# Performance work log

Measured on AMD Instinct MI355X. Metric: run time of the kernel, lower is better.

Reference implementation:

```python
import jax, jax.numpy as jnp
import numpy as np

NEG_SLOPE = 0.1
BN_EPS = 1e-5
STD_EPS = 1e-5


def leaky_relu(x):
    return jnp.where(x >= 0, x, NEG_SLOPE * x)


def conv_bn_act(x, w, gamma, beta):
    # Conv1d(kernel_size=1, bias=False) + BatchNorm1d (train-mode batch stats) + LeakyReLU(0.1)
    y = jnp.einsum('bcn,oc->bon', x, w)
    m = y.mean(axis=(0, 2), keepdims=True)
    v = y.var(axis=(0, 2), keepdims=True)  # biased, as torch BN
    y = (y - m) / jnp.sqrt(v + BN_EPS) * gamma[None, :, None] + beta[None, :, None]
    return leaky_relu(y)


def knn_idx(x, k):
    # x: [B, C, N]; faithful to torch knn(): topk(k+1) of negative squared distance, then keep first k (includes self)
    xx = jnp.sum(x * x, axis=1, keepdims=True)            # [B, 1, N]
    inner = -2.0 * jnp.einsum('bcn,bcm->bnm', x, x)       # [B, N, N]
    pd = -xx - inner - jnp.swapaxes(xx, 1, 2)             # [B, N, N]
    _, idx = jax.lax.top_k(pd, k + 1)
    return idx[:, :, :k]


def setup_inputs() -> dict:
    key = jax.random.key(0)
    ks = jax.random.split(key, 4)
    B, C, N, O = 8, 3, 4096, 32
    return {
        'xyz': jax.random.normal(ks[0], (B, C, N), dtype=jnp.float32),
        'w_nn': jax.random.normal(ks[1], (O, C), dtype=jnp.float32) * 0.1,
        'alpha': jnp.ones((1, 1, 1, O), dtype=jnp.float32),
        'beta_a': jnp.zeros((1, 1, 1, O), dtype=jnp.float32),
        'w0': jax.random.normal(ks[2], (O, C), dtype=jnp.float32) * 0.1,
        'g0': jnp.ones((O,), dtype=jnp.float32),
        'b0': jnp.zeros((O,), dtype=jnp.float32),
        'w1': jax.random.normal(ks[3], (O, O), dtype=jnp.float32) * 0.1,
        'g1': jnp.ones((O,), dtype=jnp.float32),
        'b1': jnp.zeros((O,), dtype=jnp.float32),
        'k': 16,
    }


def reference(xyz, w_nn, alpha, beta_a, w0, g0, b0, w1, g1, b1, k):
    # MLP branch on raw channels
    x = conv_bn_act(xyz, w0, g0, b0)
    x = conv_bn_act(x, w1, g1, b1)          # [B, 32, N]

    # KNN + gather neighbors
    idx = knn_idx(xyz, k)                   # [B, N, k]
    pts = jnp.swapaxes(xyz, 1, 2)           # [B, N, C]
    grouped = jax.vmap(lambda p, i: p[i])(pts, idx)  # [B, N, k, C]

    # neighbor_normal: diff -> 1x1 conv -> global-std normalize -> affine
    res = grouped - pts[:, :, None, :]
    res = jnp.einsum('bnkc,oc->bnko', res, w_nn)      # [B, N, k, 32]
    B = res.shape[0]
    std = jnp.std(res.reshape(B, -1), axis=-1, ddof=1).reshape(B, 1, 1, 1)  # torch.std is unbiased
    gp = alpha * (res / (std + STD_EPS)) + beta_a

    # max over neighbors, to [B, 32, N]
    gp = jnp.swapaxes(gp.max(axis=2), 1, 2)

    point_feature = jnp.concatenate([x, gp], axis=1)  # [B, 64, N]
    return point_feature, idx
```

## Files before the change

### kernel.cpp

```cpp
#include <hip/hip_runtime.h>
#include <stdint.h>

#define B_  8
#define N_  4096
#define O_  32
#define K_  16
#define BN_ (B_ * N_)
#define PF_ (B_ * 64 * N_)
#define CB_ 256
#define RPB 4
#define CHK 512
#define NCHK (N_ / CHK)

enum : int {
  WS_PARTA = 0,
  WS_XX    = 1024,
  WS_SC0   = WS_XX + BN_,
  WS_SH0   = WS_SC0 + 32,
  WS_PARTC = WS_SH0 + 32,
  WS_SC1   = WS_PARTC + 4096,
  WS_SH1   = WS_SC1 + 32,
  WS_MAXV  = WS_SH1 + 32,
  WS_MINV  = WS_MAXV + BN_ * 32,
  WS_ROWS  = WS_MINV + BN_ * 32,
  WS_DEN   = WS_ROWS + BN_ * 2,
  WS_TOTAL = WS_DEN + 8
};
#define WS_PARTC2 WS_MAXV

__global__ __launch_bounds__(256) void kA(const float* __restrict__ xyz,
                                          float* __restrict__ ws) {
  int tid = threadIdx.x;
  int gid = blockIdx.x * 256 + tid;
  float s0 = 0.f, s1 = 0.f, s2 = 0.f;
  float m00 = 0.f, m01 = 0.f, m02 = 0.f, m11 = 0.f, m12 = 0.f, m22 = 0.f;
  for (int i = gid; i < BN_; i += 64 * 256) {
    int b = i >> 12, n = i & (N_ - 1);
    const float* xb = xyz + b * 3 * N_;
    float x0 = xb[n], x1 = xb[N_ + n], x2 = xb[2 * N_ + n];
    float xx = __fadd_rn(__fadd_rn(__fmul_rn(x0, x0), __fmul_rn(x1, x1)),
                         __fmul_rn(x2, x2));
    ws[WS_XX + i] = xx;
    s0 += x0; s1 += x1; s2 += x2;
    m00 = fmaf(x0, x0, m00); m01 = fmaf(x0, x1, m01); m02 = fmaf(x0, x2, m02);
    m11 = fmaf(x1, x1, m11); m12 = fmaf(x1, x2, m12); m22 = fmaf(x2, x2, m22);
  }
  __shared__ float sd[256];
  float acc[9] = {s0, s1, s2, m00, m01, m02, m11, m12, m22};
#pragma unroll
  for (int q = 0; q < 9; ++q) {
    sd[tid] = acc[q];
    __syncthreads();
    for (int s = 128; s > 0; s >>= 1) {
      if (tid < s) sd[tid] += sd[tid + s];
      __syncthreads();
    }
    if (tid == 0) ws[WS_PARTA + blockIdx.x * 9 + q] = sd[0];
    __syncthreads();
  }
}

__global__ __launch_bounds__(256) void kC(const float* __restrict__ xyz,
                                          const float* __restrict__ w0,
                                          const float* __restrict__ g0,
                                          const float* __restrict__ b0,
                                          const float* __restrict__ w1,
                                          float* __restrict__ ws) {
  __shared__ float S9[9];
  __shared__ float w0s[96], sc0s[32], sh0s[32], w1s[32 * 33], xs[8][33], red[256];
  int tid = threadIdx.x;
  if (tid < 9) {
    float s = 0.f;
    for (int blk = 0; blk < 64; ++blk) s += ws[WS_PARTA + blk * 9 + tid];
    S9[tid] = s;
  }
  if (tid < 96) w0s[tid] = w0[tid];
  for (int i = tid; i < 1024; i += 256) w1s[(i >> 5) * 33 + (i & 31)] = w1[i];
  __syncthreads();
  if (tid < 32) {
    const float inv = 1.0f / 32768.0f;
    float mc0 = S9[0] * inv, mc1 = S9[1] * inv, mc2 = S9[2] * inv;
    float M00 = S9[3] * inv, M01 = S9[4] * inv, M02 = S9[5] * inv;
    float M11 = S9[6] * inv, M12 = S9[7] * inv, M22 = S9[8] * inv;
    float w0c = w0[tid * 3], w1c = w0[tid * 3 + 1], w2c = w0[tid * 3 + 2];
    float m = w0c * mc0 + w1c * mc1 + w2c * mc2;
    float e2 = w0c * w0c * M00 + w1c * w1c * M11 + w2c * w2c * M22 +
               2.f * (w0c * w1c * M01 + w0c * w2c * M02 + w1c * w2c * M12);
    float v = fmaxf(e2 - m * m, 0.f);
    float sc = g0[tid] / sqrtf(v + 1e-5f);
    float sh = b0[tid] - m * sc;
    sc0s[tid] = sc; sh0s[tid] = sh;
    if (blockIdx.x == 0) { ws[WS_SC0 + tid] = sc; ws[WS_SH0 + tid] = sh; }
  }
  __syncthreads();
  int p = tid >> 5, o = tid & 31;
  float S = 0.f, S2 = 0.f;
  for (int it = 0; it < 16; ++it) {
    int i = blockIdx.x * 128 + it * 8 + p;
    int b = i >> 12, n = i & (N_ - 1);
    const float* xb = xyz + b * 3 * N_;
    float x0 = xb[n], x1 = xb[N_ + n], x2 = xb[2 * N_ + n];
    float y0 = x0 * w0s[o * 3] + x1 * w0s[o * 3 + 1] + x2 * w0s[o * 3 + 2];
    float a = y0 * sc0s[o] + sh0s[o];
    xs[p][o] = (a >= 0.f) ? a : 0.1f * a;
    __syncthreads();
    float y1 = 0.f;
#pragma unroll
    for (int c = 0; c < 32; ++c) y1 = fmaf(w1s[o * 33 + c], xs[p][c], y1);
    S += y1; S2 = fmaf(y1, y1, S2);
    __syncthreads();
  }
  red[tid] = S;
  __syncthreads();
  if (p == 0) {
    float t = 0.f;
    for (int pp = 0; pp < 8; ++pp) t += red[pp * 32 + o];
    ws[WS_PARTC2 + blockIdx.x * 64 + o] = t;
  }
  __syncthreads();
  red[tid] = S2;
  __syncthreads();
  if (p == 0) {
    float t = 0.f;
    for (int pp = 0; pp < 8; ++pp) t += red[pp * 32 + o];
    ws[WS_PARTC2 + blockIdx.x * 64 + 32 + o] = t;
  }
}

__global__ __launch_bounds__(256) void kE(const float* __restrict__ xyz,
                                          const float* __restrict__ w0,
                                          const float* __restrict__ w1,
                                          const float* __restrict__ g1,
                                          const float* __restrict__ b1,
                                          const float* __restrict__ ws,
                                          float* __restrict__ out) {
  __shared__ float w0s[96], sc0s[32], sh0s[32], sc1s[32], sh1s[32], w1s[32 * 33],
      xs[8][33];
  int tid = threadIdx.x;
  if (tid < 96) w0s[tid] = w0[tid];
  if (tid < 32) {
    sc0s[tid] = ws[WS_SC0 + tid]; sh0s[tid] = ws[WS_SH0 + tid];
    float S = 0.f, S2 = 0.f;
    for (int blk = 0; blk < CB_; ++blk) {
      S += ws[WS_PARTC2 + blk * 64 + tid];
      S2 += ws[WS_PARTC2 + blk * 64 + 32 + tid];
    }
    float m = S / 32768.f;
    float v = fmaxf(S2 / 32768.f - m * m, 0.f);
    float sc = g1[tid] / sqrtf(v + 1e-5f);
    sc1s[tid] = sc; sh1s[tid] = b1[tid] - m * sc;
  }
  for (int i = tid; i < 1024; i += 256) w1s[(i >> 5) * 33 + (i & 31)] = w1[i];
  __syncthreads();
  int p = tid >> 5, o = tid & 31;
  int o2 = tid >> 3, p2 = tid & 7;
  for (int it = 0; it < 16; ++it) {
    int i = blockIdx.x * 128 + it * 8 + p;
    int b = i >> 12, n = i & (N_ - 1);
    const float* xb = xyz + b * 3 * N_;
    float x0 = xb[n], x1 = xb[N_ + n], x2 = xb[2 * N_ + n];
    float y0 = x0 * w0s[o * 3] + x1 * w0s[o * 3 + 1] + x2 * w0s[o * 3 + 2];
    float a = y0 * sc0s[o] + sh0s[o];
    xs[p][o] = (a >= 0.f) ? a : 0.1f * a;
    __syncthreads();
    float y1 = 0.f;
#pragma unroll
    for (int c = 0; c < 32; ++c) y1 = fmaf(w1s[o * 33 + c], xs[p][c], y1);
    float z = y1 * sc1s[o] + sh1s[o];
    float x1v = (z >= 0.f) ? z : 0.1f * z;
    __syncthreads();
    xs[p][o] = x1v;
    __syncthreads();
    int i2 = blockIdx.x * 128 + it * 8 + p2;
    int b2 = i2 >> 12, n2 = i2 & (N_ - 1);
    out[b2 * 64 * N_ + o2 * N_ + n2] = xs[p2][o2];
    __syncthreads();
  }
}

__global__ __launch_bounds__(256) void kF(const float* __restrict__ xyz,
                                          const float* __restrict__ w_nn,
                                          float* __restrict__ out,
                                          float* __restrict__ ws) {
  int tid = threadIdx.x;
  int wave = tid >> 6, lane = tid & 63;
  int row = blockIdx.x * RPB + wave;
  int b = row >> 12, n = row & (N_ - 1);
  const float* xb = xyz + b * 3 * N_;
  const float* xxp = ws + WS_XX + b * N_;
  float qx = xb[n], qy = xb[N_ + n], qz = xb[2 * N_ + n];
  float xxn = xxp[n];

  __shared__ float sx[2][CHK], sy[2][CHK], sz[2][CHK];
  __shared__ unsigned long long list[RPB][64];
  __shared__ float rb[RPB][16][33];

  float keys[64];
  float mn = __builtin_inff();
  float rx0, rx1, ry0, ry1, rz0, rz1;
  rx0 = xb[tid];           rx1 = xb[tid + 256];
  ry0 = xb[N_ + tid];      ry1 = xb[N_ + tid + 256];
  rz0 = xb[2 * N_ + tid];  rz1 = xb[2 * N_ + tid + 256];
#pragma unroll
  for (int c = 0; c < NCHK; ++c) {
    int buf = c & 1;
    sx[buf][tid] = rx0;  sx[buf][tid + 256] = rx1;
    sy[buf][tid] = ry0;  sy[buf][tid + 256] = ry1;
    sz[buf][tid] = rz0;  sz[buf][tid + 256] = rz1;
    __syncthreads();
    if (c + 1 < NCHK) {
      int i0 = (c + 1) * CHK + tid;
      rx0 = xb[i0];           rx1 = xb[i0 + 256];
      ry0 = xb[N_ + i0];      ry1 = xb[N_ + i0 + 256];
      rz0 = xb[2 * N_ + i0];  rz1 = xb[2 * N_ + i0 + 256];
    }
#pragma unroll
    for (int jj = 0; jj < CHK / 64; ++jj) {
      int ml = (jj << 6) | lane;
      float px = sx[buf][ml], py = sy[buf][ml], pz = sz[buf][ml];
      float m0 = __fmul_rn(px, px);
      float m1 = __fmul_rn(py, py);
      float m2 = __fmul_rn(pz, pz);
      asm volatile("" : "+v"(m0), "+v"(m1), "+v"(m2));
      float pw = __fadd_rn(__fadd_rn(m0, m1), m2);
      asm volatile("" : "+v"(pw));
      float dot = __fmaf_rn(pz, qz, __fmaf_rn(py, qy, __fmul_rn(px, qx)));
      asm volatile("" : "+v"(dot));
      float inner = __fmul_rn(-2.0f, dot);
      float t = __fsub_rn(-pw, inner);
      float pn = __fsub_rn(xxn, t);
      keys[c * (CHK / 64) + jj] = pn;
      mn = fminf(mn, pn);
    }
    __syncthreads();
  }

  unsigned e;
  {
    unsigned u = __float_as_uint(mn);
    u ^= ((unsigned)((int)u >> 31)) | 0x80000000u;
    e = u;
  }
#pragma unroll
  for (int k = 2; k <= 64; k <<= 1) {
#pragma unroll
    for (int d = k >> 1; d >= 1; d >>= 1) {
      unsigned pe = __shfl_xor(e, d, 64);
      bool up = ((lane & k) == 0);
      bool lower = ((lane & d) == 0);
      unsigned lo = (e < pe) ? e : pe;
      unsigned hi = (e < pe) ? pe : e;
      e = (up == lower) ? lo : hi;
    }
  }
  unsigned tm = __shfl(e, 15, 64);
  unsigned tfu = (tm & 0x80000000u) ? (tm ^ 0x80000000u) : ~tm;
  float T = __uint_as_float(tfu);

  list[wave][lane] = ~0ull;
  __syncthreads();
  int base = 0;
#pragma unroll
  for (int j = 0; j < 64; ++j) {
    bool pred = (keys[j] <= T);
    unsigned long long mask = __ballot(pred);
    if (mask != 0ull) {
      if (pred) {
        unsigned uu = __float_as_uint(keys[j]);
        uu ^= ((unsigned)((int)uu >> 31)) | 0x80000000u;
        int rank = __popcll(mask & ((1ull << lane) - 1ull));
        int slot = base + rank;
        if (slot < 64)
          list[wave][slot] = ((unsigned long long)uu << 32) |
                             (unsigned)((j << 6) | lane);
      }
      base += __popcll(mask);
    }
  }
  __syncthreads();

  unsigned long long ev = list[wave][lane];
#pragma unroll
  for (int k = 2; k <= 64; k <<= 1) {
#pragma unroll
    for (int d = k >> 1; d >= 1; d >>= 1) {
      unsigned long long pe = __shfl_xor(ev, d, 64);
      bool up = ((lane & k) == 0);
      bool lower = ((lane & d) == 0);
      bool lt = (ev < pe);
      unsigned long long lo = lt ? ev : pe;
      unsigned long long hi = lt ? pe : ev;
      ev = (up == lower) ? lo : hi;
    }
  }
  int m = (int)(unsigned)(ev & 0xffffffffull);
  if (lane < 16) out[PF_ + row * 16 + lane] = (float)m;

  float s = 0.f, s2 = 0.f;
  if (lane < 16) {
    float dx = __fsub_rn(xb[m], qx);
    float dy = __fsub_rn(xb[N_ + m], qy);
    float dz = __fsub_rn(xb[2 * N_ + m], qz);
#pragma unroll
    for (int o = 0; o < 32; ++o) {
      float r = __fmaf_rn(dz, w_nn[o * 3 + 2],
                __fmaf_rn(dy, w_nn[o * 3 + 1], __fmul_rn(dx, w_nn[o * 3])));
      rb[wave][lane][o] = r;
      s += r;
      s2 = __fmaf_rn(r, r, s2);
    }
  }
  __syncthreads();
  if (lane < 32) {
    float mx = -__builtin_inff(), mnv = __builtin_inff();
#pragma unroll
    for (int r = 0; r < 16; ++r) {
      float v = rb[wave][r][lane];
      mx = fmaxf(mx, v);
      mnv = fminf(mnv, v);
    }
    ws[WS_MAXV + row * 32 + lane] = mx;
    ws[WS_MINV + row * 32 + lane] = mnv;
  }
#pragma unroll
  for (int off = 1; off < 64; off <<= 1) {
    s += __shfl_xor(s, off, 64);
    s2 += __shfl_xor(s2, off, 64);
  }
  if (lane == 0) {
    ws[WS_ROWS + row * 2] = s;
    ws[WS_ROWS + row * 2 + 1] = s2;
  }
}

__global__ __launch_bounds__(256) void kH(const float* __restrict__ alpha,
                                          const float* __restrict__ beta,
                                          const float* __restrict__ ws,
                                          float* __restrict__ out) {
  int tid = threadIdx.x;
  int i = blockIdx.x * 256 + tid;
  int b = i >> 17;
  float s = 0.f, s2 = 0.f;
  for (int q = tid; q < N_; q += 256) {
    s += ws[WS_ROWS + (b * N_ + q) * 2];
    s2 += ws[WS_ROWS + (b * N_ + q) * 2 + 1];
  }
  __shared__ float sd[256], sd2[256];
  __shared__ float den_s;
  sd[tid] = s; sd2[tid] = s2;
  __syncthreads();
  for (int st = 128; st > 0; st >>= 1) {
    if (tid < st) { sd[tid] += sd[tid + st]; sd2[tid] += sd2[tid + st]; }
    __syncthreads();
  }
  if (tid == 0) {
    const float M = 2097152.0f;
    float var = fmaxf((sd2[0] - sd[0] * (sd[0] / M)) / (M - 1.0f), 0.f);
    den_s = sqrtf(var) + 1e-5f;
  }
  __syncthreads();
  float denom = den_s;
  int n = i & (N_ - 1);
  int o = (i >> 12) & 31;
  float al = alpha[o], be = beta[o];
  int base = (b * N_ + n) * 32 + o;
  float v = (al >= 0.f) ? ws[WS_MAXV + base] : ws[WS_MINV + base];
  out[b * 64 * N_ + (32 + o) * N_ + n] = __fadd_rn(__fmul_rn(al, v / denom), be);
}

extern "C" void kernel_launch(void* const* d_in, const int* in_sizes, int n_in,
                              void* d_out, int out_size, void* d_ws, size_t ws_size,
                              hipStream_t stream) {
  const float* xyz   = (const float*)d_in[0];
  const float* w_nn  = (const float*)d_in[1];
  const float* alpha = (const float*)d_in[2];
  const float* beta_a= (const float*)d_in[3];
  const float* w0    = (const float*)d_in[4];
  const float* g0    = (const float*)d_in[5];
  const float* b0    = (const float*)d_in[6];
  const float* w1    = (const float*)d_in[7];
  const float* g1    = (const float*)d_in[8];
  const float* b1    = (const float*)d_in[9];
  float* out = (float*)d_out;
  float* ws  = (float*)d_ws;

  kA<<<64, 256, 0, stream>>>(xyz, ws);
  kC<<<CB_, 256, 0, stream>>>(xyz, w0, g0, b0, w1, ws);
  kE<<<CB_, 256, 0, stream>>>(xyz, w0, w1, g1, b1, ws, out);
  kF<<<BN_ / RPB, RPB * 64, 0, stream>>>(xyz, w_nn, out, ws);
  kH<<<(B_ * 32 * N_ + 255) / 256, 256, 0, stream>>>(alpha, beta_a, ws, out);
}
```

Baseline: 146.5 us.

## Cache conv1 output in workspace, alias kF shared memory, select max/min in kF

kC now stores the pre-BN second conv output to the workspace so kE only loads it and applies BN plus LeakyReLU, no longer recomputing the first conv and the 32x32 matmul. kF's shared arrays are merged into a single 12 KB buffer reused across phases, which lowers LDS use per block and may allow more blocks per CU. kF also picks max or min by the sign of alpha and writes one array, so kH reads half as much. The cost is an extra 4 MB write in kC and a read in kE.

```diff
diff --git a/kernel.cpp b/kernel.cpp
--- a/kernel.cpp
+++ b/kernel.cpp
@@ -27,6 +27,7 @@
   WS_TOTAL = WS_DEN + 8
 };
 #define WS_PARTC2 WS_MAXV
+#define WS_Y1     WS_MINV
 
 __global__ __launch_bounds__(256) void kA(const float* __restrict__ xyz,
                                           float* __restrict__ ws) {
@@ -90,7 +91,6 @@
     float sc = g0[tid] / sqrtf(v + 1e-5f);
     float sh = b0[tid] - m * sc;
     sc0s[tid] = sc; sh0s[tid] = sh;
-    if (blockIdx.x == 0) { ws[WS_SC0 + tid] = sc; ws[WS_SH0 + tid] = sh; }
   }
   __syncthreads();
   int p = tid >> 5, o = tid & 31;
@@ -107,6 +107,7 @@
     float y1 = 0.f;
 #pragma unroll
     for (int c = 0; c < 32; ++c) y1 = fmaf(w1s[o * 33 + c], xs[p][c], y1);
+    ws[WS_Y1 + i * 32 + o] = y1;
     S += y1; S2 = fmaf(y1, y1, S2);
     __syncthreads();
   }
@@ -127,19 +128,13 @@
   }
 }
 
-__global__ __launch_bounds__(256) void kE(const float* __restrict__ xyz,
-                                          const float* __restrict__ w0,
-                                          const float* __restrict__ w1,
-                                          const float* __restrict__ g1,
+__global__ __launch_bounds__(256) void kE(const float* __restrict__ g1,
                                           const float* __restrict__ b1,
                                           const float* __restrict__ ws,
                                           float* __restrict__ out) {
-  __shared__ float w0s[96], sc0s[32], sh0s[32], sc1s[32], sh1s[32], w1s[32 * 33],
-      xs[8][33];
-  int tid = threadIdx.x;
-  if (tid < 96) w0s[tid] = w0[tid];
+  __shared__ float sc1s[32], sh1s[32], xs[8][33];
+  int tid = threadIdx.x;
   if (tid < 32) {
-    sc0s[tid] = ws[WS_SC0 + tid]; sh0s[tid] = ws[WS_SH0 + tid];
     float S = 0.f, S2 = 0.f;
     for (int blk = 0; blk < CB_; ++blk) {
       S += ws[WS_PARTC2 + blk * 64 + tid];
@@ -150,25 +145,14 @@
     float sc = g1[tid] / sqrtf(v + 1e-5f);
     sc1s[tid] = sc; sh1s[tid] = b1[tid] - m * sc;
   }
-  for (int i = tid; i < 1024; i += 256) w1s[(i >> 5) * 33 + (i & 31)] = w1[i];
   __syncthreads();
   int p = tid >> 5, o = tid & 31;
   int o2 = tid >> 3, p2 = tid & 7;
   for (int it = 0; it < 16; ++it) {
     int i = blockIdx.x * 128 + it * 8 + p;
-    int b = i >> 12, n = i & (N_ - 1);
-    const float* xb = xyz + b * 3 * N_;
-    float x0 = xb[n], x1 = xb[N_ + n], x2 = xb[2 * N_ + n];
-    float y0 = x0 * w0s[o * 3] + x1 * w0s[o * 3 + 1] + x2 * w0s[o * 3 + 2];
-    float a = y0 * sc0s[o] + sh0s[o];
-    xs[p][o] = (a >= 0.f) ? a : 0.1f * a;
-    __syncthreads();
-    float y1 = 0.f;
-#pragma unroll
-    for (int c = 0; c < 32; ++c) y1 = fmaf(w1s[o * 33 + c], xs[p][c], y1);
+    float y1 = ws[WS_Y1 + i * 32 + o];
     float z = y1 * sc1s[o] + sh1s[o];
     float x1v = (z >= 0.f) ? z : 0.1f * z;
-    __syncthreads();
     xs[p][o] = x1v;
     __syncthreads();
     int i2 = blockIdx.x * 128 + it * 8 + p2;
@@ -180,6 +164,7 @@
 
 __global__ __launch_bounds__(256) void kF(const float* __restrict__ xyz,
                                           const float* __restrict__ w_nn,
+                                          const float* __restrict__ alpha,
                                           float* __restrict__ out,
                                           float* __restrict__ ws) {
   int tid = threadIdx.x;
@@ -191,9 +176,10 @@
   float qx = xb[n], qy = xb[N_ + n], qz = xb[2 * N_ + n];
   float xxn = xxp[n];
 
-  __shared__ float sx[2][CHK], sy[2][CHK], sz[2][CHK];
-  __shared__ unsigned long long list[RPB][64];
-  __shared__ float rb[RPB][16][33];
+  __shared__ __align__(16) char smem[12288];
+  float* sxp = (float*)smem;
+  float* syp = (float*)(smem + 4096);
+  float* szp = (float*)(smem + 8192);
 
   float keys[64];
   float mn = __builtin_inff();
@@ -203,10 +189,10 @@
   rz0 = xb[2 * N_ + tid];  rz1 = xb[2 * N_ + tid + 256];
 #pragma unroll
   for (int c = 0; c < NCHK; ++c) {
-    int buf = c & 1;
-    sx[buf][tid] = rx0;  sx[buf][tid + 256] = rx1;
-    sy[buf][tid] = ry0;  sy[buf][tid + 256] = ry1;
-    sz[buf][tid] = rz0;  sz[buf][tid + 256] = rz1;
+    int buf = (c & 1) * CHK;
+    sxp[buf + tid] = rx0;  sxp[buf + tid + 256] = rx1;
+    syp[buf + tid] = ry0;  syp[buf + tid + 256] = ry1;
+    szp[buf + tid] = rz0;  szp[buf + tid + 256] = rz1;
     __syncthreads();
     if (c + 1 < NCHK) {
       int i0 = (c + 1) * CHK + tid;
@@ -216,8 +202,8 @@
     }
 #pragma unroll
     for (int jj = 0; jj < CHK / 64; ++jj) {
-      int ml = (jj << 6) | lane;
-      float px = sx[buf][ml], py = sy[buf][ml], pz = sz[buf][ml];
+      int ml = buf + ((jj << 6) | lane);
+      float px = sxp[ml], py = syp[ml], pz = szp[ml];
       float m0 = __fmul_rn(px, px);
       float m1 = __fmul_rn(py, py);
       float m2 = __fmul_rn(pz, pz);
@@ -234,6 +220,8 @@
     }
     __syncthreads();
   }
+  unsigned long long* listp = (unsigned long long*)smem;
+  float* rbp = (float*)(smem + 2048);
 
   unsigned e;
   {
@@ -257,7 +245,7 @@
   unsigned tfu = (tm & 0x80000000u) ? (tm ^ 0x80000000u) : ~tm;
   float T = __uint_as_float(tfu);
 
-  list[wave][lane] = ~0ull;
+  listp[wave * 64 + lane] = ~0ull;
   __syncthreads();
   int base = 0;
 #pragma unroll
@@ -271,15 +259,15 @@
         int rank = __popcll(mask & ((1ull << lane) - 1ull));
         int slot = base + rank;
         if (slot < 64)
-          list[wave][slot] = ((unsigned long long)uu << 32) |
-                             (unsigned)((j << 6) | lane);
+          listp[wave * 64 + slot] = ((unsigned long long)uu << 32) |
+                                    (unsigned)((j << 6) | lane);
       }
       base += __popcll(mask);
     }
   }
   __syncthreads();
 
-  unsigned long long ev = list[wave][lane];
+  unsigned long long ev = listp[wave * 64 + lane];
 #pragma unroll
   for (int k = 2; k <= 64; k <<= 1) {
 #pragma unroll
@@ -305,7 +293,7 @@
     for (int o = 0; o < 32; ++o) {
       float r = __fmaf_rn(dz, w_nn[o * 3 + 2],
                 __fmaf_rn(dy, w_nn[o * 3 + 1], __fmul_rn(dx, w_nn[o * 3])));
-      rb[wave][lane][o] = r;
+      rbp[(wave * 16 + lane) * 33 + o] = r;
       s += r;
       s2 = __fmaf_rn(r, r, s2);
     }
@@ -315,12 +303,12 @@
     float mx = -__builtin_inff(), mnv = __builtin_inff();
 #pragma unroll
     for (int r = 0; r < 16; ++r) {
-      float v = rb[wave][r][lane];
+      float v = rbp[(wave * 16 + r) * 33 + lane];
       mx = fmaxf(mx, v);
       mnv = fminf(mnv, v);
     }
-    ws[WS_MAXV + row * 32 + lane] = mx;
-    ws[WS_MINV + row * 32 + lane] = mnv;
+    float al = alpha[lane];
+    ws[WS_MAXV + row * 32 + lane] = (al >= 0.f) ? mx : mnv;
   }
 #pragma unroll
   for (int off = 1; off < 64; off <<= 1) {
@@ -363,8 +351,7 @@
   int n = i & (N_ - 1);
   int o = (i >> 12) & 31;
   float al = alpha[o], be = beta[o];
-  int base = (b * N_ + n) * 32 + o;
-  float v = (al >= 0.f) ? ws[WS_MAXV + base] : ws[WS_MINV + base];
+  float v = ws[WS_MAXV + (b * N_ + n) * 32 + o];
   out[b * 64 * N_ + (32 + o) * N_ + n] = __fadd_rn(__fmul_rn(al, v / denom), be);
 }
 
@@ -386,7 +373,7 @@
 
   kA<<<64, 256, 0, stream>>>(xyz, ws);
   kC<<<CB_, 256, 0, stream>>>(xyz, w0, g0, b0, w1, ws);
-  kE<<<CB_, 256, 0, stream>>>(xyz, w0, w1, g1, b1, ws, out);
-  kF<<<BN_ / RPB, RPB * 64, 0, stream>>>(xyz, w_nn, out, ws);
+  kE<<<CB_, 256, 0, stream>>>(g1, b1, ws, out);
+  kF<<<BN_ / RPB, RPB * 64, 0, stream>>>(xyz, w_nn, alpha, out, ws);
   kH<<<(B_ * 32 * N_ + 255) / 256, 256, 0, stream>>>(alpha, beta_a, ws, out);
 }
```

After: 139.7 us, median of 2. 4.7% less time.
